# Optimization experiments

Hardware: AMD Instinct MI355X
Metric: run time of the kernel (lower is better)

Reference implementation:

```python
import jax, jax.numpy as jnp
import numpy as np

N, D, F, O = 32768, 32, 128, 128  # nodes, fixed in-degree, in_feats, out_feats


def _lstm_reduce(m, W_ih, W_hh, b_ih, b_hh):
    """Run an LSTM over each node's neighbor mailbox m: [N, T, F] -> final h: [N, H].
    PyTorch gate order: i, f, g, o. W_ih: [4H, F], W_hh: [4H, H]."""
    n, _, _ = m.shape
    H = W_hh.shape[1]
    b = b_ih + b_hh

    def step(carry, x_t):
        h, c = carry
        gates = x_t @ W_ih.T + h @ W_hh.T + b  # [N, 4H]
        i, f, g, o = jnp.split(gates, 4, axis=-1)
        c = jax.nn.sigmoid(f) * c + jax.nn.sigmoid(i) * jnp.tanh(g)
        h = jax.nn.sigmoid(o) * jnp.tanh(c)
        return (h, c), None

    h0 = jnp.zeros((n, H), m.dtype)
    (h_final, _), _ = jax.lax.scan(step, (h0, h0), jnp.swapaxes(m, 0, 1))
    return h_final


def setup_inputs() -> dict:
    key = jax.random.key(0)
    ks = jax.random.split(key, 9)
    stdv_lin = 1.0 / np.sqrt(F)   # linear init: uniform(-1/sqrt(in_feats))
    stdv_lstm = 1.0 / np.sqrt(F)  # torch LSTM init: uniform(-1/sqrt(hidden))
    u = lambda k, shape, s: jax.random.uniform(k, shape, jnp.float32, -s, s)
    return {
        "feat": jax.random.normal(ks[0], (N, F), jnp.float32),
        "neigh_idx": jax.random.randint(ks[1], (N, D), 0, N, jnp.int32),
        "W_ih": u(ks[2], (4 * F, F), stdv_lstm),
        "W_hh": u(ks[3], (4 * F, F), stdv_lstm),
        "b_ih": u(ks[4], (4 * F,), stdv_lstm),
        "b_hh": u(ks[5], (4 * F,), stdv_lstm),
        "W1": u(ks[6], (O, F), stdv_lin),
        "b1": u(ks[6], (O,), stdv_lin),
        "W2": u(ks[7], (O, F), stdv_lin),
        "b2": u(ks[8], (O,), stdv_lin),
    }


def reference(feat, neigh_idx, W_ih, W_hh, b_ih, b_hh, W1, b1, W2, b2):
    # Mailbox gather: each node's D neighbor feature rows -> [N, D, F]
    m = feat[neigh_idx]
    # LSTM reducer -> final hidden state per node
    h = _lstm_reduce(m, W_ih, W_hh, b_ih, b_hh)  # [N, F]
    degs = jnp.asarray(neigh_idx.shape[1], feat.dtype)  # fixed-degree graph
    ah = h / degs
    # feat = linear1(feat) + linear2(ah)
    return feat @ W1.T + b1 + ah @ W2.T + b2
```

## Files before the change

### kernel.cpp

```cpp
#include <hip/hip_runtime.h>
#include <hip/hip_bf16.h>

#define NN 32768
#define DEG 32
#define FF 128
#define OO 128
#define MB 32

typedef __attribute__((ext_vector_type(8))) short bfrag;
typedef __attribute__((ext_vector_type(4))) float f32x4;

#define K1 1.4426950408889634f

__device__ __forceinline__ unsigned short b16(float x) {
    unsigned u = __float_as_uint(x) + 0x8000u;
    return (unsigned short)(u >> 16);
}
__device__ __forceinline__ bfrag pack8(float4 a, float4 b) {
    bfrag r;
    r[0] = (short)b16(a.x); r[1] = (short)b16(a.y); r[2] = (short)b16(a.z); r[3] = (short)b16(a.w);
    r[4] = (short)b16(b.x); r[5] = (short)b16(b.y); r[6] = (short)b16(b.z); r[7] = (short)b16(b.w);
    return r;
}

__device__ __forceinline__ float fsig(float x, float nb) {
    return __builtin_amdgcn_rcpf(1.0f + __builtin_amdgcn_exp2f(fmaf(-K1, x, nb)));
}
__device__ __forceinline__ float ftanh_b(float x, float pb) {
    return fmaf(-2.0f, __builtin_amdgcn_rcpf(1.0f + __builtin_amdgcn_exp2f(fmaf(2.0f * K1, x, pb))), 1.0f);
}
__device__ __forceinline__ float ftanh(float x) {
    return fmaf(-2.0f, __builtin_amdgcn_rcpf(1.0f + __builtin_amdgcn_exp2f(2.0f * K1 * x)), 1.0f);
}

__global__ void prep_weights(const float* __restrict__ wih, const float* __restrict__ whh,
                             const float* __restrict__ b_ih, const float* __restrict__ b_hh,
                             const float* __restrict__ w1, const float* __restrict__ b1,
                             const float* __restrict__ w2, const float* __restrict__ b2,
                             short* __restrict__ wihb, short* __restrict__ whhb,
                             short* __restrict__ w1b, short* __restrict__ w2b,
                             float* __restrict__ biasg, float* __restrict__ biaso)
{
    int i = blockIdx.x * blockDim.x + threadIdx.x;
    if (i < 512 * 128) { wihb[i] = (short)b16(wih[i]); whhb[i] = (short)b16(whh[i]); }
    if (i < 128 * 128) { w1b[i] = (short)b16(w1[i]); w2b[i] = (short)b16(w2[i] * 0.03125f); }
    if (i < 512) biasg[i] = b_ih[i] + b_hh[i];
    if (i < 128) biaso[i] = b1[i] + b2[i];
}

__global__ void prep_feat(const float* __restrict__ f, short* __restrict__ fb) {
    int i = blockIdx.x * blockDim.x + threadIdx.x;
    const float4* p = reinterpret_cast<const float4*>(f) + (size_t)i * 2;
    float4 a = p[0], b = p[1];
    *reinterpret_cast<bfrag*>(fb + (size_t)i * 8) = pack8(a, b);
}

template<bool BF16F>
__device__ __forceinline__ bfrag load_row8(const float* __restrict__ ff, const short* __restrict__ fb,
                                           int node, int cs) {
    if (BF16F) {
        return *reinterpret_cast<const bfrag*>(fb + node * FF + cs * 8);
    } else {
        const float4* p = reinterpret_cast<const float4*>(ff + node * FF + cs * 8);
        return pack8(p[0], p[1]);
    }
}

template<bool BF16F>
__global__ __launch_bounds__(512, 2)
void sage_lstm_kernel(const float* __restrict__ featf, const short* __restrict__ featb,
                      const int* __restrict__ nidx,
                      const short* __restrict__ wihb, const short* __restrict__ whhb,
                      const short* __restrict__ w1b, const short* __restrict__ w2b,
                      const float* __restrict__ biasg, const float* __restrict__ biaso,
                      float* __restrict__ out)
{
    __shared__ short xbuf[2][MB * 128];
    __shared__ short hbuf[2][MB * 128];
    __shared__ int   idx_s[MB * DEG];

    const int tid  = (int)threadIdx.x;
    const int lane = tid & 63;
    const int wave = tid >> 6;
    const int n0   = (int)blockIdx.x * MB;

    const int srow = tid >> 4;
    const int cs   = tid & 15;

    idx_s[tid]       = nidx[n0 * DEG + tid];
    idx_s[512 + tid] = nidx[n0 * DEG + 512 + tid];
    {   bfrag z; for (int j = 0; j < 8; ++j) z[j] = 0;
        reinterpret_cast<bfrag*>(hbuf[0])[tid] = z; }

    const int colw = wave * 16 + (lane & 15);
    bfrag wih[4][4], whh[4][4];
#pragma unroll
    for (int g = 0; g < 4; ++g) {
        const short* pih = wihb + (g * 128 + colw) * FF + (lane >> 4) * 8;
        const short* phh = whhb + (g * 128 + colw) * FF + (lane >> 4) * 8;
#pragma unroll
        for (int kt = 0; kt < 4; ++kt) {
            wih[g][kt] = *reinterpret_cast<const bfrag*>(pih + kt * 32);
            whh[g][kt] = *reinterpret_cast<const bfrag*>(phh + kt * 32);
        }
    }
    const float nbi = -K1 * biasg[colw];
    const float nbf = -K1 * biasg[128 + colw];
    const float pbg = 2.0f * K1 * biasg[256 + colw];
    const float nbo = -K1 * biasg[384 + colw];

    __syncthreads();

    {
        bfrag v = load_row8<BF16F>(featf, featb, idx_s[srow * DEG], cs);
        int sb = (srow * 256 + cs * 16) ^ ((srow & 7) << 4);
        *reinterpret_cast<bfrag*>(reinterpret_cast<char*>(xbuf[0]) + sb) = v;
    }
    __syncthreads();

    const int arow = lane & 15;
    const int asub = (lane >> 4) * 16;
    const int hr0  = (lane >> 4) * 4;
    const int par  = wave & 1;
    f32x4 cs0 = {0.f, 0.f, 0.f, 0.f};
    f32x4 cs1 = {0.f, 0.f, 0.f, 0.f};

    for (int t = 0; t < DEG; ++t) {
        const int cur = t & 1;
        char* xcur = reinterpret_cast<char*>(xbuf[cur]);
        char* hcur = reinterpret_cast<char*>(hbuf[cur]);
        char* xnxt = reinterpret_cast<char*>(xbuf[cur ^ 1]);
        char* hnxt = reinterpret_cast<char*>(hbuf[cur ^ 1]);

        bfrag pre;
        if (t < DEG - 1) pre = load_row8<BF16F>(featf, featb, idx_s[srow * DEG + t + 1], cs);

        auto do_rt = [&](int rt, f32x4& cst) {
            const int rowr = rt * 16 + arow;
            const int sw   = (rowr & 7) << 4;
            bfrag xa[4], ha[4];
#pragma unroll
            for (int kt = 0; kt < 4; ++kt) {
                int byte = (rowr * 256 + kt * 64 + asub) ^ sw;
                xa[kt] = *reinterpret_cast<const bfrag*>(xcur + byte);
                ha[kt] = *reinterpret_cast<const bfrag*>(hcur + byte);
            }
            f32x4 gi = {0,0,0,0}, gf = {0,0,0,0}, gg = {0,0,0,0}, go = {0,0,0,0};
            __builtin_amdgcn_s_setprio(1);
#pragma unroll
            for (int kt = 0; kt < 4; ++kt) {
                gi = __builtin_amdgcn_mfma_f32_16x16x32_bf16(xa[kt], wih[0][kt], gi, 0, 0, 0);
                gf = __builtin_amdgcn_mfma_f32_16x16x32_bf16(xa[kt], wih[1][kt], gf, 0, 0, 0);
                gg = __builtin_amdgcn_mfma_f32_16x16x32_bf16(xa[kt], wih[2][kt], gg, 0, 0, 0);
                go = __builtin_amdgcn_mfma_f32_16x16x32_bf16(xa[kt], wih[3][kt], go, 0, 0, 0);
            }
#pragma unroll
            for (int kt = 0; kt < 4; ++kt) {
                gi = __builtin_amdgcn_mfma_f32_16x16x32_bf16(ha[kt], whh[0][kt], gi, 0, 0, 0);
                gf = __builtin_amdgcn_mfma_f32_16x16x32_bf16(ha[kt], whh[1][kt], gf, 0, 0, 0);
                gg = __builtin_amdgcn_mfma_f32_16x16x32_bf16(ha[kt], whh[2][kt], gg, 0, 0, 0);
                go = __builtin_amdgcn_mfma_f32_16x16x32_bf16(ha[kt], whh[3][kt], go, 0, 0, 0);
            }
            __builtin_amdgcn_s_setprio(0);
#pragma unroll
            for (int r = 0; r < 4; ++r) {
                float iv = fsig(gi[r], nbi);
                float fv = fsig(gf[r], nbf);
                float gv = ftanh_b(gg[r], pbg);
                float ov = fsig(go[r], nbo);
                float c  = fmaf(fv, cst[r], iv * gv);
                cst[r] = c;
                float h  = ov * ftanh(c);
                int hrow = rt * 16 + hr0 + r;
                int hb   = (hrow * 256 + colw * 2) ^ ((hrow & 7) << 4);
                *reinterpret_cast<unsigned short*>(hnxt + hb) = b16(h);
            }
        };

        if (par == 0) { do_rt(0, cs0); do_rt(1, cs1); }
        else          { do_rt(1, cs1); do_rt(0, cs0); }

        if (t < DEG - 1) {
            int sb = (srow * 256 + cs * 16) ^ ((srow & 7) << 4);
            *reinterpret_cast<bfrag*>(xnxt + sb) = pre;
        }
        __syncthreads();
    }

    {
        bfrag v = load_row8<BF16F>(featf, featb, n0 + srow, cs);
        int sb = (srow * 256 + cs * 16) ^ ((srow & 7) << 4);
        *reinterpret_cast<bfrag*>(reinterpret_cast<char*>(xbuf[0]) + sb) = v;
    }
    __syncthreads();

    bfrag w1f[4], w2f[4];
#pragma unroll
    for (int kt = 0; kt < 4; ++kt) {
        w1f[kt] = *reinterpret_cast<const bfrag*>(w1b + colw * FF + kt * 32 + (lane >> 4) * 8);
        w2f[kt] = *reinterpret_cast<const bfrag*>(w2b + colw * FF + kt * 32 + (lane >> 4) * 8);
    }
    const float bb = biaso[colw];
#pragma unroll
    for (int rt = 0; rt < 2; ++rt) {
        const int rowr = rt * 16 + arow;
        const int sw   = (rowr & 7) << 4;
        bfrag fa[4], hfa[4];
#pragma unroll
        for (int kt = 0; kt < 4; ++kt) {
            int byte = (rowr * 256 + kt * 64 + asub) ^ sw;
            fa[kt]  = *reinterpret_cast<const bfrag*>(reinterpret_cast<char*>(xbuf[0]) + byte);
            hfa[kt] = *reinterpret_cast<const bfrag*>(reinterpret_cast<char*>(hbuf[0]) + byte);
        }
        f32x4 acc = {0.f, 0.f, 0.f, 0.f};
#pragma unroll
        for (int kt = 0; kt < 4; ++kt) {
            acc = __builtin_amdgcn_mfma_f32_16x16x32_bf16(fa[kt],  w1f[kt], acc, 0, 0, 0);
            acc = __builtin_amdgcn_mfma_f32_16x16x32_bf16(hfa[kt], w2f[kt], acc, 0, 0, 0);
        }
#pragma unroll
        for (int r = 0; r < 4; ++r) {
            int orow = n0 + rt * 16 + hr0 + r;
            out[orow * OO + colw] = acc[r] + bb;
        }
    }
}

extern "C" void kernel_launch(void* const* d_in, const int* in_sizes, int n_in,
                              void* d_out, int out_size, void* d_ws, size_t ws_size,
                              hipStream_t stream)
{
    const float* feat = (const float*)d_in[0];
    const int*   nidx = (const int*)d_in[1];
    const float* W_ih = (const float*)d_in[2];
    const float* W_hh = (const float*)d_in[3];
    const float* b_ih = (const float*)d_in[4];
    const float* b_hh = (const float*)d_in[5];
    const float* W1   = (const float*)d_in[6];
    const float* b1   = (const float*)d_in[7];
    const float* W2   = (const float*)d_in[8];
    const float* b2   = (const float*)d_in[9];
    float* out = (float*)d_out;

    char* ws = (char*)d_ws;
    short* wihb  = (short*)(ws);
    short* whhb  = (short*)(ws + 131072);
    short* w1b   = (short*)(ws + 262144);
    short* w2b   = (short*)(ws + 294912);
    float* biasg = (float*)(ws + 327680);
    float* biaso = (float*)(ws + 329728);
    short* featb = (short*)(ws + 330240);

    const size_t need = 330240 + (size_t)NN * FF * 2;
    const bool bf = ws_size >= need;

    prep_weights<<<256, 256, 0, stream>>>(W_ih, W_hh, b_ih, b_hh, W1, b1, W2, b2,
                                          wihb, whhb, w1b, w2b, biasg, biaso);
    if (bf) {
        prep_feat<<<2048, 256, 0, stream>>>(feat, featb);
        sage_lstm_kernel<true><<<NN / MB, 512, 0, stream>>>(feat, featb, nidx, wihb, whhb,
                                                            w1b, w2b, biasg, biaso, out);
    } else {
        sage_lstm_kernel<false><<<NN / MB, 512, 0, stream>>>(feat, featb, nidx, wihb, whhb,
                                                             w1b, w2b, biasg, biaso, out);
    }
}
```

Before: 328.6 us.

## Software-pipeline LSTM input projection and use direct global-to-LDS neighbor loads

Restructures the recurrence so the input projection x_{t+1}·W_ih is computed during step t alongside the hidden projection, using double sets of gate accumulators. This takes the input matmul off the serial h-dependency chain. Neighbor rows are now staged two steps ahead with global_load_lds (direct-to-LDS async copies) instead of going through registers. The cost is roughly double the accumulator registers, which may pressure occupancy under the 512x2 launch bounds.

```diff
diff --git a/kernel.cpp b/kernel.cpp
--- a/kernel.cpp
+++ b/kernel.cpp
@@ -26,11 +26,17 @@
 __device__ __forceinline__ float fsig(float x, float nb) {
     return __builtin_amdgcn_rcpf(1.0f + __builtin_amdgcn_exp2f(fmaf(-K1, x, nb)));
 }
-__device__ __forceinline__ float ftanh_b(float x, float pb) {
+__device__ __forceinline__ float ftanhb(float x, float pb) {
     return fmaf(-2.0f, __builtin_amdgcn_rcpf(1.0f + __builtin_amdgcn_exp2f(fmaf(2.0f * K1, x, pb))), 1.0f);
 }
 __device__ __forceinline__ float ftanh(float x) {
     return fmaf(-2.0f, __builtin_amdgcn_rcpf(1.0f + __builtin_amdgcn_exp2f(2.0f * K1 * x)), 1.0f);
+}
+
+__device__ __forceinline__ void gload16(const void* g, void* l) {
+    __builtin_amdgcn_global_load_lds(
+        (const __attribute__((address_space(1))) unsigned int*)g,
+        (__attribute__((address_space(3))) unsigned int*)l, 16, 0, 0);
 }
 
 __global__ void prep_weights(const float* __restrict__ wih, const float* __restrict__ whh,
@@ -56,17 +62,6 @@
 }
 
 template<bool BF16F>
-__device__ __forceinline__ bfrag load_row8(const float* __restrict__ ff, const short* __restrict__ fb,
-                                           int node, int cs) {
-    if (BF16F) {
-        return *reinterpret_cast<const bfrag*>(fb + node * FF + cs * 8);
-    } else {
-        const float4* p = reinterpret_cast<const float4*>(ff + node * FF + cs * 8);
-        return pack8(p[0], p[1]);
-    }
-}
-
-template<bool BF16F>
 __global__ __launch_bounds__(512, 2)
 void sage_lstm_kernel(const float* __restrict__ featf, const short* __restrict__ featb,
                       const int* __restrict__ nidx,
@@ -86,6 +81,7 @@
 
     const int srow = tid >> 4;
     const int cs   = tid & 15;
+    const int chunk = (cs ^ (srow & 7)) * 8;
 
     idx_s[tid]       = nidx[n0 * DEG + tid];
     idx_s[512 + tid] = nidx[n0 * DEG + 512 + tid];
@@ -111,86 +107,117 @@
 
     __syncthreads();
 
-    {
-        bfrag v = load_row8<BF16F>(featf, featb, idx_s[srow * DEG], cs);
+    char* const x0p = reinterpret_cast<char*>(xbuf[0]);
+    char* const x1p = reinterpret_cast<char*>(xbuf[1]);
+    char* const h0p = reinterpret_cast<char*>(hbuf[0]);
+    char* const h1p = reinterpret_cast<char*>(hbuf[1]);
+
+    if (BF16F) {
+        gload16(featb + idx_s[srow * DEG + 0] * FF + chunk, x0p + wave * 1024);
+        gload16(featb + idx_s[srow * DEG + 1] * FF + chunk, x1p + wave * 1024);
+    } else {
         int sb = (srow * 256 + cs * 16) ^ ((srow & 7) << 4);
-        *reinterpret_cast<bfrag*>(reinterpret_cast<char*>(xbuf[0]) + sb) = v;
+        {   const float4* p = reinterpret_cast<const float4*>(featf + idx_s[srow * DEG + 0] * FF + cs * 8);
+            *reinterpret_cast<bfrag*>(x0p + sb) = pack8(p[0], p[1]); }
+        {   const float4* p = reinterpret_cast<const float4*>(featf + idx_s[srow * DEG + 1] * FF + cs * 8);
+            *reinterpret_cast<bfrag*>(x1p + sb) = pack8(p[0], p[1]); }
     }
     __syncthreads();
 
     const int arow = lane & 15;
     const int asub = (lane >> 4) * 16;
     const int hr0  = (lane >> 4) * 4;
-    const int par  = wave & 1;
-    f32x4 cs0 = {0.f, 0.f, 0.f, 0.f};
-    f32x4 cs1 = {0.f, 0.f, 0.f, 0.f};
-
-    for (int t = 0; t < DEG; ++t) {
-        const int cur = t & 1;
-        char* xcur = reinterpret_cast<char*>(xbuf[cur]);
-        char* hcur = reinterpret_cast<char*>(hbuf[cur]);
-        char* xnxt = reinterpret_cast<char*>(xbuf[cur ^ 1]);
-        char* hnxt = reinterpret_cast<char*>(hbuf[cur ^ 1]);
-
-        bfrag pre;
-        if (t < DEG - 1) pre = load_row8<BF16F>(featf, featb, idx_s[srow * DEG + t + 1], cs);
-
-        auto do_rt = [&](int rt, f32x4& cst) {
-            const int rowr = rt * 16 + arow;
-            const int sw   = (rowr & 7) << 4;
-            bfrag xa[4], ha[4];
-#pragma unroll
-            for (int kt = 0; kt < 4; ++kt) {
-                int byte = (rowr * 256 + kt * 64 + asub) ^ sw;
-                xa[kt] = *reinterpret_cast<const bfrag*>(xcur + byte);
-                ha[kt] = *reinterpret_cast<const bfrag*>(hcur + byte);
-            }
-            f32x4 gi = {0,0,0,0}, gf = {0,0,0,0}, gg = {0,0,0,0}, go = {0,0,0,0};
-            __builtin_amdgcn_s_setprio(1);
-#pragma unroll
-            for (int kt = 0; kt < 4; ++kt) {
-                gi = __builtin_amdgcn_mfma_f32_16x16x32_bf16(xa[kt], wih[0][kt], gi, 0, 0, 0);
-                gf = __builtin_amdgcn_mfma_f32_16x16x32_bf16(xa[kt], wih[1][kt], gf, 0, 0, 0);
-                gg = __builtin_amdgcn_mfma_f32_16x16x32_bf16(xa[kt], wih[2][kt], gg, 0, 0, 0);
-                go = __builtin_amdgcn_mfma_f32_16x16x32_bf16(xa[kt], wih[3][kt], go, 0, 0, 0);
-            }
-#pragma unroll
-            for (int kt = 0; kt < 4; ++kt) {
-                gi = __builtin_amdgcn_mfma_f32_16x16x32_bf16(ha[kt], whh[0][kt], gi, 0, 0, 0);
-                gf = __builtin_amdgcn_mfma_f32_16x16x32_bf16(ha[kt], whh[1][kt], gf, 0, 0, 0);
-                gg = __builtin_amdgcn_mfma_f32_16x16x32_bf16(ha[kt], whh[2][kt], gg, 0, 0, 0);
-                go = __builtin_amdgcn_mfma_f32_16x16x32_bf16(ha[kt], whh[3][kt], go, 0, 0, 0);
-            }
-            __builtin_amdgcn_s_setprio(0);
-#pragma unroll
-            for (int r = 0; r < 4; ++r) {
-                float iv = fsig(gi[r], nbi);
-                float fv = fsig(gf[r], nbf);
-                float gv = ftanh_b(gg[r], pbg);
-                float ov = fsig(go[r], nbo);
-                float c  = fmaf(fv, cst[r], iv * gv);
-                cst[r] = c;
-                float h  = ov * ftanh(c);
-                int hrow = rt * 16 + hr0 + r;
-                int hb   = (hrow * 256 + colw * 2) ^ ((hrow & 7) << 4);
-                *reinterpret_cast<unsigned short*>(hnxt + hb) = b16(h);
-            }
-        };
-
-        if (par == 0) { do_rt(0, cs0); do_rt(1, cs1); }
-        else          { do_rt(1, cs1); do_rt(0, cs0); }
-
-        if (t < DEG - 1) {
+    const int swz  = (arow & 7) << 4;
+
+    auto mm4 = [&](const char* p, int rbase, const bfrag (&W)[4][4],
+                   f32x4& vi, f32x4& vf, f32x4& vg, f32x4& vo) {
+        bfrag a[4];
+#pragma unroll
+        for (int kt = 0; kt < 4; ++kt)
+            a[kt] = *reinterpret_cast<const bfrag*>(p + ((rbase * 256 + kt * 64 + asub) ^ swz));
+#pragma unroll
+        for (int kt = 0; kt < 4; ++kt) {
+            vi = __builtin_amdgcn_mfma_f32_16x16x32_bf16(a[kt], W[0][kt], vi, 0, 0, 0);
+            vf = __builtin_amdgcn_mfma_f32_16x16x32_bf16(a[kt], W[1][kt], vf, 0, 0, 0);
+            vg = __builtin_amdgcn_mfma_f32_16x16x32_bf16(a[kt], W[2][kt], vg, 0, 0, 0);
+            vo = __builtin_amdgcn_mfma_f32_16x16x32_bf16(a[kt], W[3][kt], vo, 0, 0, 0);
+        }
+    };
+
+    auto actw = [&](f32x4& gi, f32x4& gf, f32x4& gg, f32x4& go,
+                    f32x4& cst, char* hnxt, int rt) {
+#pragma unroll
+        for (int r = 0; r < 4; ++r) {
+            float iv = fsig(gi[r], nbi);
+            float fv = fsig(gf[r], nbf);
+            float gv = ftanhb(gg[r], pbg);
+            float ov = fsig(go[r], nbo);
+            float c  = fmaf(fv, cst[r], iv * gv);
+            cst[r] = c;
+            float h  = ov * ftanh(c);
+            int hrow = rt * 16 + hr0 + r;
+            int hb   = (hrow * 256 + colw * 2) ^ ((hrow & 7) << 4);
+            *reinterpret_cast<unsigned short*>(hnxt + hb) = b16(h);
+        }
+    };
+
+    auto stage = [&](int t, char* xwr) {
+        int node = idx_s[srow * DEG + t];
+        if (BF16F) {
+            gload16(featb + node * FF + chunk, xwr + wave * 1024);
+        } else {
+            const float4* p = reinterpret_cast<const float4*>(featf + node * FF + cs * 8);
             int sb = (srow * 256 + cs * 16) ^ ((srow & 7) << 4);
-            *reinterpret_cast<bfrag*>(xnxt + sb) = pre;
-        }
-        __syncthreads();
-    }
-
-    {
-        bfrag v = load_row8<BF16F>(featf, featb, n0 + srow, cs);
+            *reinterpret_cast<bfrag*>(xwr + sb) = pack8(p[0], p[1]);
+        }
+    };
+
+    const f32x4 zz = {0.f, 0.f, 0.f, 0.f};
+    f32x4 cs0 = zz, cs1 = zz;
+
+    f32x4 Ai0, Af0, Ag0, Ao0, Ai1, Af1, Ag1, Ao1;
+    f32x4 Bi0, Bf0, Bg0, Bo0, Bi1, Bf1, Bg1, Bo1;
+
+    Ai0 = zz; Af0 = zz; Ag0 = zz; Ao0 = zz;
+    mm4(x0p, arow, wih, Ai0, Af0, Ag0, Ao0);
+    Ai1 = zz; Af1 = zz; Ag1 = zz; Ao1 = zz;
+    mm4(x0p, 16 + arow, wih, Ai1, Af1, Ag1, Ao1);
+    __syncthreads();
+
+#define STEP(T, Gi0,Gf0,Gg0,Go0, Gi1,Gf1,Gg1,Go1, Pi0,Pf0,Pg0,Po0, Pi1,Pf1,Pg1,Po1, HCUR,HNXT,XRD,XWR) \
+    {                                                                                  \
+        if ((T) < DEG - 2) stage((T) + 2, XWR);                                        \
+        __builtin_amdgcn_s_setprio(1);                                                 \
+        mm4(HCUR, arow, whh, Gi0, Gf0, Gg0, Go0);                                      \
+        if ((T) < DEG - 1) {                                                           \
+            Pi0 = zz; Pf0 = zz; Pg0 = zz; Po0 = zz;                                    \
+            mm4(XRD, arow, wih, Pi0, Pf0, Pg0, Po0);                                   \
+        }                                                                              \
+        mm4(HCUR, 16 + arow, whh, Gi1, Gf1, Gg1, Go1);                                 \
+        if ((T) < DEG - 1) {                                                           \
+            Pi1 = zz; Pf1 = zz; Pg1 = zz; Po1 = zz;                                    \
+            mm4(XRD, 16 + arow, wih, Pi1, Pf1, Pg1, Po1);                              \
+        }                                                                              \
+        __builtin_amdgcn_s_setprio(0);                                                 \
+        actw(Gi0, Gf0, Gg0, Go0, cs0, HNXT, 0);                                        \
+        actw(Gi1, Gf1, Gg1, Go1, cs1, HNXT, 1);                                        \
+        __syncthreads();                                                               \
+    }
+
+    for (int tt = 0; tt < DEG; tt += 2) {
+        STEP(tt,     Ai0,Af0,Ag0,Ao0, Ai1,Af1,Ag1,Ao1,
+                     Bi0,Bf0,Bg0,Bo0, Bi1,Bf1,Bg1,Bo1, h0p, h1p, x1p, x0p);
+        STEP(tt + 1, Bi0,Bf0,Bg0,Bo0, Bi1,Bf1,Bg1,Bo1,
+                     Ai0,Af0,Ag0,Ao0, Ai1,Af1,Ag1,Ao1, h1p, h0p, x0p, x1p);
+    }
+#undef STEP
+
+    if (BF16F) {
+        gload16(featb + (n0 + srow) * FF + chunk, x0p + wave * 1024);
+    } else {
+        const float4* p = reinterpret_cast<const float4*>(featf + (n0 + srow) * FF + cs * 8);
         int sb = (srow * 256 + cs * 16) ^ ((srow & 7) << 4);
-        *reinterpret_cast<bfrag*>(reinterpret_cast<char*>(xbuf[0]) + sb) = v;
+        *reinterpret_cast<bfrag*>(x0p + sb) = pack8(p[0], p[1]);
     }
     __syncthreads();
 
@@ -204,13 +231,12 @@
 #pragma unroll
     for (int rt = 0; rt < 2; ++rt) {
         const int rowr = rt * 16 + arow;
-        const int sw   = (rowr & 7) << 4;
         bfrag fa[4], hfa[4];
 #pragma unroll
         for (int kt = 0; kt < 4; ++kt) {
-            int byte = (rowr * 256 + kt * 64 + asub) ^ sw;
-            fa[kt]  = *reinterpret_cast<const bfrag*>(reinterpret_cast<char*>(xbuf[0]) + byte);
-            hfa[kt] = *reinterpret_cast<const bfrag*>(reinterpret_cast<char*>(hbuf[0]) + byte);
+            int byte = (rowr * 256 + kt * 64 + asub) ^ swz;
+            fa[kt]  = *reinterpret_cast<const bfrag*>(x0p + byte);
+            hfa[kt] = *reinterpret_cast<const bfrag*>(h0p + byte);
         }
         f32x4 acc = {0.f, 0.f, 0.f, 0.f};
 #pragma unroll
@@ -218,9 +244,10 @@
             acc = __builtin_amdgcn_mfma_f32_16x16x32_bf16(fa[kt],  w1f[kt], acc, 0, 0, 0);
             acc = __builtin_amdgcn_mfma_f32_16x16x32_bf16(hfa[kt], w2f[kt], acc, 0, 0, 0);
         }
+        const int hr0e = (lane >> 4) * 4;
 #pragma unroll
         for (int r = 0; r < 4; ++r) {
-            int orow = n0 + rt * 16 + hr0 + r;
+            int orow = n0 + rt * 16 + hr0e + r;
             out[orow * OO + colw] = acc[r] + bb;
         }
     }
```

After: 326.1 us. Within noise of the previous version (-0.8%).
